# Kernel optimization log

Hardware: AMD Instinct MI355X
Metric: run time of the kernel (lower is better)

## Reference

```python
import jax, jax.numpy as jnp
import numpy as np

OBS, ACT, H, B = 128, 32, 64, 32768
TMAX = 8  # max variable-length GRU steps: (15-1)//2+1 == 15//2+1 == 8
CENTER = 7


def gru_last(x_seq, valid, Wih, Whh, bih, bhh):
    """torch nn.GRU cell, masked scan; returns final hidden at each true length.
    x_seq: (B, TMAX, D), valid: (B, TMAX) bool. Gate order r, z, n."""
    Bn = x_seq.shape[0]
    h0 = jnp.zeros((Bn, Whh.shape[1]), x_seq.dtype)

    def step(h, inp):
        xt, vt = inp  # (B, D), (B,)
        gi = xt @ Wih.T + bih
        gh = h @ Whh.T + bhh
        ir, iz, inn = jnp.split(gi, 3, axis=-1)
        hr, hz, hn = jnp.split(gh, 3, axis=-1)
        r = jax.nn.sigmoid(ir + hr)
        zg = jax.nn.sigmoid(iz + hz)
        n = jnp.tanh(inn + r * hn)
        hnew = (1.0 - zg) * n + zg * h
        h = jnp.where(vt[:, None], hnew, h)
        return h, None

    h, _ = jax.lax.scan(step, h0, (jnp.swapaxes(x_seq, 0, 1), valid.T))
    return h


def setup_inputs() -> dict:
    key = jax.random.key(0)
    ks = jax.random.split(key, 20)
    def p(k, shape, s=0.05):
        return jax.random.normal(k, shape, jnp.float32) * s
    D = OBS + ACT
    return dict(
        obs_chunk=jax.random.normal(ks[0], (B, 15, OBS), jnp.float32),
        act_chunk=jax.random.normal(ks[1], (B, 15, ACT), jnp.float32),
        ln_g=jnp.ones((3,), jnp.float32), ln_b=jnp.zeros((3,), jnp.float32),
        dw1=p(ks[2], (16, 3)), db1=jnp.zeros((16,), jnp.float32),
        dw2=p(ks[3], (8, 16)), db2=jnp.zeros((8,), jnp.float32),
        dw3=p(ks[4], (14, 8)), db3=jnp.zeros((14,), jnp.float32),
        Wih_f=p(ks[5], (3 * H, D)), Whh_f=p(ks[6], (3 * H, H)),
        bih_f=jnp.zeros((3 * H,), jnp.float32), bhh_f=jnp.zeros((3 * H,), jnp.float32),
        Wih_b=p(ks[7], (3 * H, D)), Whh_b=p(ks[8], (3 * H, H)),
        bih_b=jnp.zeros((3 * H,), jnp.float32), bhh_b=jnp.zeros((3 * H,), jnp.float32),
        mw1=p(ks[9], (H, 2 * H)), mb1=jnp.zeros((H,), jnp.float32),
        mw2=p(ks[10], (H, H)), mb2=jnp.zeros((H,), jnp.float32),
        mu_w=p(ks[11], (H, H)), mu_b=jnp.zeros((H,), jnp.float32),
        lv_w=p(ks[12], (H, H)), lv_b=jnp.zeros((H,), jnp.float32),
    )


def reference(obs_chunk, act_chunk, ln_g, ln_b, dw1, db1, dw2, db2, dw3, db3,
              Wih_f, Whh_f, bih_f, bhh_f, Wih_b, Whh_b, bih_b, bhh_b,
              mw1, mb1, mw2, mb2, mu_w, mu_b, lv_w, lv_b):
    C = CENTER
    # --- DynamicTimeWindow features ---
    obs_t = obs_chunk[:, C]  # (B, OBS)
    pr = jax.nn.softmax(obs_t, axis=-1)
    entropy = -jnp.sum(pr * jnp.log(pr + 1e-8), axis=-1, keepdims=True)
    diffs = jnp.stack([jnp.linalg.norm(obs_chunk[:, C - k] - obs_chunk[:, C - k - 1], axis=-1)
                       for k in range(3)], axis=1)
    roc = diffs.mean(axis=1, keepdims=True)
    act_prev = act_chunk[:, C - 1]
    md = max(obs_t.shape[-1], act_prev.shape[-1])
    op = jnp.pad(obs_t, ((0, 0), (0, md - obs_t.shape[-1])))
    ap = jnp.pad(act_prev, ((0, 0), (0, md - act_prev.shape[-1])))
    oc = op - op.mean(axis=1, keepdims=True)
    ac = ap - ap.mean(axis=1, keepdims=True)
    denom = (jnp.linalg.norm(oc, axis=1, keepdims=True)
             * jnp.linalg.norm(ac, axis=1, keepdims=True) + 1e-8)
    corr = jnp.sum(oc * ac, axis=1, keepdims=True) / denom
    f = jnp.concatenate([entropy, roc, corr], axis=1)  # (B, 3)
    mean = f.mean(axis=-1, keepdims=True)
    var = f.var(axis=-1, keepdims=True)  # biased, matches torch LayerNorm
    fn = (f - mean) / jnp.sqrt(var + 1e-5) * ln_g + ln_b
    h1 = jax.nn.relu(fn @ dw1.T + db1)
    h2 = jax.nn.relu(h1 @ dw2.T + db2)
    logits = h2 @ dw3.T + db3  # (B, 14)
    widx = jnp.argmax(logits, axis=1)  # test_mode: argmax of softmax == argmax of logits
    wl = widx + 2  # window_len in [2, 15]
    idxs = jnp.arange(15)[None, :]
    start = (C - (wl - 1) // 2)[:, None]
    end = (C + wl // 2 + 1)[:, None]
    mask = ((idxs >= start) & (idxs < end)).astype(obs_chunk.dtype)  # (B, 15)
    x = jnp.concatenate([obs_chunk, act_chunk], axis=-1) * mask[..., None]  # (B, 15, D)
    # --- BiGRU over variable-length windows ---
    len_f = (wl - 1) // 2 + 1  # (B,)
    len_b = wl // 2 + 1
    t = jnp.arange(TMAX)
    idx_f = C - len_f[:, None] + 1 + t[None, :]  # left-aligned forward window
    idx_b = C + len_b[:, None] - 1 - t[None, :]  # reversed backward window
    seq_f = jnp.take_along_axis(x, idx_f[..., None], axis=1)  # (B, 8, D)
    seq_b = jnp.take_along_axis(x, idx_b[..., None], axis=1)
    vf = t[None, :] < len_f[:, None]
    vb = t[None, :] < len_b[:, None]
    h_f = gru_last(seq_f, vf, Wih_f, Whh_f, bih_f, bhh_f)  # (B, H)
    h_b = gru_last(seq_b, vb, Wih_b, Whh_b, bih_b, bhh_b)
    comb = jnp.concatenate([h_f, h_b], axis=1)  # (B, 2H)
    zenc = jax.nn.relu(comb @ mw1.T + mb1) @ mw2.T + mb2
    mu = zenc @ mu_w.T + mu_b
    sigma = jnp.exp(0.5 * (zenc @ lv_w.T + lv_b))
    z = mu  # test_mode=True
    return (z, mu, sigma)
```

## Files before the change

kernel.cpp:

```cpp
#include <hip/hip_runtime.h>

#define OBS 128
#define ACTD 32
#define DIMX 160
#define HID 64
#define NBATCH 32768
#define TMAXX 8
#define CTR 7
#define NPOS 15

typedef short bf16x8 __attribute__((ext_vector_type(8)));
typedef float f32x4 __attribute__((ext_vector_type(4)));

#define MFMA(a,b,c) __builtin_amdgcn_mfma_f32_16x16x32_bf16((a),(b),(c),0,0,0)

#define CTRL_BYTE 262144
#define SIDX_BYTE 278528
#define SIDX_CAP  66048
#define WB_BYTE   542720
#define COMB_BYTE 755712
#define NCB 64
#define EPB 512
#define BH_OFF (40 + 1024)
#define HEAD_W_OFF 10752
#define TOTAL_SLOTS 13312

__device__ __forceinline__ unsigned short f2bf(float f) {
  unsigned u = __float_as_uint(f);
  return (unsigned short)((u + 0x7FFFu + ((u >> 16) & 1u)) >> 16);
}
__device__ __forceinline__ unsigned cvtpk(float a, float b) {
  unsigned r;
  asm("v_cvt_pk_bf16_f32 %0, %1, %2" : "=v"(r) : "v"(a), "v"(b));
  return r;
}

__device__ __forceinline__ float wsum(float v) {
#pragma unroll
  for (int s = 1; s < 64; s <<= 1) v += __shfl_xor(v, s);
  return v;
}
__device__ __forceinline__ float wmax(float v) {
#pragma unroll
  for (int s = 1; s < 64; s <<= 1) v = fmaxf(v, __shfl_xor(v, s));
  return v;
}

__global__ __launch_bounds__(256) void k_decide(
    const float* __restrict__ obs, const float* __restrict__ act,
    const float* __restrict__ ln_g, const float* __restrict__ ln_b,
    const float* __restrict__ dw1, const float* __restrict__ db1,
    const float* __restrict__ dw2, const float* __restrict__ db2,
    const float* __restrict__ dw3, const float* __restrict__ db3,
    int* __restrict__ lens) {
  int b = blockIdx.x * 4 + (threadIdx.x >> 6);
  int l = threadIdx.x & 63;
  const float* o7 = obs + ((size_t)b * NPOS + CTR) * OBS;
  const float* o6 = o7 - OBS;
  const float* o5 = o7 - 2 * OBS;
  const float* o4 = o7 - 3 * OBS;
  float x0 = o7[l], x1 = o7[l + 64];
  float y60 = o6[l], y61 = o6[l + 64];
  float y50 = o5[l], y51 = o5[l + 64];
  float y40 = o4[l], y41 = o4[l + 64];
  float ap = (l < 32) ? act[((size_t)b * NPOS + 6) * ACTD + l] : 0.0f;

  float m = wmax(fmaxf(x0, x1));
  float e0 = __expf(x0 - m), e1 = __expf(x1 - m);
  float s = wsum(e0 + e1);
  float dot = wsum(e0 * (x0 - m) + e1 * (x1 - m));
  float ent = __logf(s) - dot / s;

  float d0 = wsum((x0 - y60) * (x0 - y60) + (x1 - y61) * (x1 - y61));
  float d1 = wsum((y60 - y50) * (y60 - y50) + (y61 - y51) * (y61 - y51));
  float d2 = wsum((y50 - y40) * (y50 - y40) + (y51 - y41) * (y51 - y41));
  float roc = (sqrtf(d0) + sqrtf(d1) + sqrtf(d2)) / 3.0f;

  float sop = wsum(x0 + x1);
  float sop2 = wsum(x0 * x0 + x1 * x1);
  float sap = wsum(ap);
  float sap2 = wsum(ap * ap);
  float dotoa = wsum(ap * x0);
  float mo = sop / 128.0f, ma = sap / 128.0f;
  float num = dotoa - 128.0f * mo * ma;
  float oc2 = fmaxf(sop2 - 128.0f * mo * mo, 0.0f);
  float ac2 = fmaxf(sap2 - 128.0f * ma * ma, 0.0f);
  float corr = num / (sqrtf(oc2) * sqrtf(ac2) + 1e-8f);

  float f0 = ent, f1 = roc, f2 = corr;
  float mean = (f0 + f1 + f2) / 3.0f;
  float v0 = f0 - mean, v1 = f1 - mean, v2 = f2 - mean;
  float var = (v0 * v0 + v1 * v1 + v2 * v2) / 3.0f;
  float sd = sqrtf(var + 1e-5f);
  float fn0 = v0 / sd * ln_g[0] + ln_b[0];
  float fn1 = v1 / sd * ln_g[1] + ln_b[1];
  float fn2 = v2 / sd * ln_g[2] + ln_b[2];

  float h1[16];
#pragma unroll
  for (int i = 0; i < 16; i++) {
    float a = db1[i] + fn0 * dw1[i * 3] + fn1 * dw1[i * 3 + 1] + fn2 * dw1[i * 3 + 2];
    h1[i] = fmaxf(a, 0.0f);
  }
  float h2[8];
#pragma unroll
  for (int i = 0; i < 8; i++) {
    float a = db2[i];
#pragma unroll
    for (int j = 0; j < 16; j++) a += h1[j] * dw2[i * 16 + j];
    h2[i] = fmaxf(a, 0.0f);
  }
  float best = -3.0e38f;
  int bi = 0;
#pragma unroll
  for (int i = 0; i < 14; i++) {
    float a = db3[i];
#pragma unroll
    for (int j = 0; j < 8; j++) a += h2[j] * dw3[i * 8 + j];
    if (a > best) { best = a; bi = i; }
  }
  int wl = bi + 2;
  if (l == 0) {
    lens[b] = (wl - 1) / 2 + 1;
    lens[NBATCH + b] = wl / 2 + 1;
  }
}

__global__ __launch_bounds__(256) void k_cp(
    const int* __restrict__ lens, int* __restrict__ ctrl,
    const float* __restrict__ Wih_f, const float* __restrict__ Whh_f,
    const float* __restrict__ Wih_b, const float* __restrict__ Whh_b,
    const float* __restrict__ mw1, const float* __restrict__ mw2,
    const float* __restrict__ mu_w, const float* __restrict__ lv_w,
    unsigned short* __restrict__ dst) {
  __shared__ int hist[16];
  const int tid = threadIdx.x, blk = blockIdx.x;
  if (tid < 16) hist[tid] = 0;
  __syncthreads();
#pragma unroll
  for (int j = 0; j < 2; j++) {
    int e = blk * EPB + j * 256 + tid;
    atomicAdd(&hist[lens[e] - 1], 1);
    atomicAdd(&hist[8 + lens[NBATCH + e] - 1], 1);
  }
  {
    int slot = blk * 208 + (tid % 208) + (tid / 208) * 13312;
    if (tid < 208) {
      const float* src;
      if (slot < HEAD_W_OFF) {
        int d = slot / 5376, r = slot % 5376;
        int f = r >> 8, rw = r & 255;
        int w = rw >> 6, lane = rw & 63;
        int col = lane & 15, kgrp = lane >> 4;
        int row = 16 * w + col;
        if (f < 15) {
          int g = f / 5, kf = f % 5;
          const float* W = d ? Wih_b : Wih_f;
          src = W + (size_t)(g * 64 + row) * 160 + kf * 32 + kgrp * 8;
        } else {
          int f2 = f - 15, g = f2 >> 1, kh = f2 & 1;
          const float* W = d ? Whh_b : Whh_f;
          src = W + (size_t)(g * 64 + row) * 64 + kh * 32 + kgrp * 8;
        }
      } else {
        int s2 = slot - HEAD_W_OFF;
        int f = s2 >> 8, rw = s2 & 255;
        int w = rw >> 6, lane = rw & 63;
        int col = lane & 15, kgrp = lane >> 4;
        int gr = 16 * w + col;
        if (f < 4)      src = mw1 + (size_t)gr * 128 + f * 32 + kgrp * 8;
        else if (f < 6) src = mw2 + (size_t)gr * 64 + (f - 4) * 32 + kgrp * 8;
        else if (f < 8) src = mu_w + (size_t)gr * 64 + (f - 6) * 32 + kgrp * 8;
        else            src = lv_w + (size_t)gr * 64 + (f - 8) * 32 + kgrp * 8;
      }
      unsigned short* o = dst + (size_t)slot * 8;
#pragma unroll
      for (int i = 0; i < 8; i++) o[i] = f2bf(src[i]);
    }
  }
  __syncthreads();
  if (tid < 16) ctrl[BH_OFF + blk * 16 + tid] = hist[tid];
}

__global__ __launch_bounds__(256) void k_scanplace(
    const int* __restrict__ lens, int* __restrict__ ctrl,
    int* __restrict__ sidx) {
  __shared__ int hist[16];
  __shared__ int base[16];
  __shared__ int tot[16];
  __shared__ int pre[16];
  __shared__ int pss[17];
  __shared__ int border[16];
  __shared__ int bstart[16];
  const int tid = threadIdx.x, blk = blockIdx.x;
  const int* bh = ctrl + BH_OFF;
  if (tid < 16) {
    int t = 0, pr = 0;
    for (int b2 = 0; b2 < NCB; b2++) {
      int h = bh[b2 * 16 + tid];
      if (b2 < blk) pr += h;
      t += h;
    }
    tot[tid] = t;
    pre[tid] = pr;
    hist[tid] = 0;
  }
  __syncthreads();
  if (tid == 0) {
    int acc = 0;
    for (int r = 0; r < 16; r++) {
      int bin = (r & 1) * 8 + 7 - (r >> 1);
      border[r] = bin;
      pss[r] = acc;
      bstart[bin] = acc;
      acc += (tot[bin] + 31) & ~31;
    }
    pss[16] = acc;
    if (blk == 0) {
      for (int r = 0; r < 17; r++) ctrl[r] = pss[r];
      for (int r = 0; r < 16; r++) ctrl[17 + r] = border[r];
    }
  }
  __syncthreads();
  if (tid < 16) base[tid] = bstart[tid] + pre[tid];
  __syncthreads();
  if (blk == 0) {
    for (int r = 0; r < 16; r++) {
      int bin = border[r];
      int s = pss[r] + tot[bin], e2 = pss[r + 1];
      for (int i = s + tid; i < e2; i += 256) sidx[i] = -1;
    }
  }
#pragma unroll
  for (int j = 0; j < 2; j++) {
    int e = blk * EPB + j * 256 + tid;
    int binf = lens[e] - 1;
    sidx[base[binf] + atomicAdd(&hist[binf], 1)] = e;
    int binb = 8 + lens[NBATCH + e] - 1;
    sidx[base[binb] + atomicAdd(&hist[binb], 1)] = e;
  }
}

__global__ __launch_bounds__(256, 2) void k_gru(
    const float* __restrict__ obs, const float* __restrict__ act,
    const int* __restrict__ ctrl, const int* __restrict__ sidx,
    const unsigned short* __restrict__ wbf,
    const float* __restrict__ bih_f, const float* __restrict__ bhh_f,
    const float* __restrict__ bih_b, const float* __restrict__ bhh_b,
    unsigned short* __restrict__ comb) {
  __shared__ unsigned short Xl[2][32 * 168];
  __shared__ unsigned short Hl[2][32 * 72];
  __shared__ int ei[32];

  const int tid = threadIdx.x;
  const int p = blockIdx.x * 32;
  if (p >= ctrl[16]) return;
  int r = 0;
#pragma unroll
  for (int k = 1; k < 16; k++) r += (p >= ctrl[k]) ? 1 : 0;
  const int bin = ctrl[17 + r];
  const int d = bin >> 3;
  const int len = (bin & 7) + 1;

  if (tid < 32) ei[tid] = sidx[p + tid];
  __syncthreads();

  const int w = tid >> 6, l = tid & 63;
  const int col = l & 15, kgrp = l >> 4;
  const int gr = 16 * w + col;

  const float* bih = d ? bih_b : bih_f;
  const float* bhh = d ? bhh_b : bhh_f;
  const float bias_r = bih[gr] + bhh[gr];
  const float bias_z = bih[64 + gr] + bhh[64 + gr];
  const float bias_in = bih[128 + gr];
  const float bias_hn = bhh[128 + gr];

  const unsigned short* fb = wbf + ((size_t)d * 5376 + tid) * 8;
  bf16x8 wr[5], wz[5], wn[5];
#pragma unroll
  for (int kf = 0; kf < 5; kf++) {
    wr[kf] = *(const bf16x8*)(fb + (size_t)kf * 2048);
    wz[kf] = *(const bf16x8*)(fb + (size_t)(5 + kf) * 2048);
    wn[kf] = *(const bf16x8*)(fb + (size_t)(10 + kf) * 2048);
  }
  bf16x8 vr[2], vz[2], vn[2];
#pragma unroll
  for (int kh = 0; kh < 2; kh++) {
    vr[kh] = *(const bf16x8*)(fb + (size_t)(15 + kh) * 2048);
    vz[kh] = *(const bf16x8*)(fb + (size_t)(17 + kh) * 2048);
    vn[kh] = *(const bf16x8*)(fb + (size_t)(19 + kh) * 2048);
  }

  const int p0 = d ? (CTR + len - 1) : (CTR - len + 1);
  const float* pst[5];
  int sstr[5], sdo[5];
#pragma unroll
  for (int it = 0; it < 5; it++) {
    int i = tid + it * 256;
    int eloc = i / 40;
    int q = i - eloc * 40;
    int eg = ei[eloc];
    if (eg < 0) eg = ei[0];
    if (q < 32) {
      pst[it] = obs + ((size_t)eg * NPOS + p0) * OBS + q * 4;
      sstr[it] = d ? -OBS : OBS;
    } else {
      pst[it] = act + ((size_t)eg * NPOS + p0) * ACTD + (q - 32) * 4;
      sstr[it] = d ? -ACTD : ACTD;
    }
    sdo[it] = eloc * 168 + ((q < 32) ? q * 4 : 128 + (q - 32) * 4);
  }
  float4 sv[5];

  auto stage_issue = [&](int t1) {
#pragma unroll
    for (int it = 0; it < 5; it++)
      sv[it] = *(const float4*)(pst[it] + (ptrdiff_t)t1 * sstr[it]);
  };
  auto stage_commit = [&](int buf) {
#pragma unroll
    for (int it = 0; it < 5; it++) {
      uint2 pk;
      pk.x = cvtpk(sv[it].x, sv[it].y);
      pk.y = cvtpk(sv[it].z, sv[it].w);
      *(uint2*)(&Xl[buf][sdo[it]]) = pk;
    }
  };

  stage_issue(0);
  stage_commit(0);
  __syncthreads();

  f32x4 hreg[2];
#pragma unroll
  for (int m = 0; m < 2; m++) hreg[m] = (f32x4){0.f, 0.f, 0.f, 0.f};

  for (int t = 0; t < len; t++) {
    const int cur = t & 1, nxt = cur ^ 1;
    const bool more = (t + 1 < len);
    if (more) stage_issue(t + 1);

    f32x4 ar[2], az[2], ain[2], ahn[2];
#pragma unroll
    for (int m = 0; m < 2; m++) {
      ar[m] = (f32x4){bias_r, bias_r, bias_r, bias_r};
      az[m] = (f32x4){bias_z, bias_z, bias_z, bias_z};
      ain[m] = (f32x4){bias_in, bias_in, bias_in, bias_in};
      ahn[m] = (f32x4){bias_hn, bias_hn, bias_hn, bias_hn};
    }
#pragma unroll
    for (int kf = 0; kf < 5; kf++) {
#pragma unroll
      for (int m = 0; m < 2; m++) {
        bf16x8 xa = *(const bf16x8*)(&Xl[cur][(col + 16 * m) * 168 + kf * 32 + kgrp * 8]);
        ar[m] = MFMA(xa, wr[kf], ar[m]);
        az[m] = MFMA(xa, wz[kf], az[m]);
        ain[m] = MFMA(xa, wn[kf], ain[m]);
      }
    }
    if (t > 0) {
#pragma unroll
      for (int kh = 0; kh < 2; kh++) {
#pragma unroll
        for (int m = 0; m < 2; m++) {
          bf16x8 ha = *(const bf16x8*)(&Hl[cur][(col + 16 * m) * 72 + kh * 32 + kgrp * 8]);
          ar[m] = MFMA(ha, vr[kh], ar[m]);
          az[m] = MFMA(ha, vz[kh], az[m]);
          ahn[m] = MFMA(ha, vn[kh], ahn[m]);
        }
      }
    }

#pragma unroll
    for (int m = 0; m < 2; m++) {
      float hvv[4];
#pragma unroll
      for (int r2 = 0; r2 < 4; r2++) {
        float rg = __builtin_amdgcn_rcpf(1.0f + __expf(-ar[m][r2]));
        float zg = __builtin_amdgcn_rcpf(1.0f + __expf(-az[m][r2]));
        float nn = fmaf(rg, ahn[m][r2], ain[m][r2]);
        float th = fmaf(-2.0f, __builtin_amdgcn_rcpf(__expf(2.0f * nn) + 1.0f), 1.0f);
        float hp = hreg[m][r2];
        float hv = fmaf(zg, hp - th, th);
        hreg[m][r2] = hv;
        hvv[r2] = hv;
      }
      if (more) {
        unsigned ua = cvtpk(hvv[0], hvv[1]);
        unsigned ub = cvtpk(hvv[2], hvv[3]);
        int row0 = (16 * m + kgrp * 4) * 72 + gr;
        Hl[nxt][row0] = (unsigned short)ua;
        Hl[nxt][row0 + 72] = (unsigned short)(ua >> 16);
        Hl[nxt][row0 + 144] = (unsigned short)ub;
        Hl[nxt][row0 + 216] = (unsigned short)(ub >> 16);
      }
    }

    if (more) {
      stage_commit(nxt);
      __syncthreads();
    }
  }

#pragma unroll
  for (int m = 0; m < 2; m++) {
#pragma unroll
    for (int r2 = 0; r2 < 4; r2++) {
      int eg = ei[16 * m + kgrp * 4 + r2];
      if (eg >= 0)
        comb[(size_t)eg * 128 + 64 * d + gr] = f2bf(hreg[m][r2]);
    }
  }
}

__global__ __launch_bounds__(256) void k_head(
    const unsigned short* __restrict__ comb, const unsigned short* __restrict__ wbf,
    const float* __restrict__ mb1, const float* __restrict__ mb2,
    const float* __restrict__ mu_b, const float* __restrict__ lv_b,
    float* __restrict__ out) {
  __shared__ unsigned short Cl[64 * 136];
  __shared__ unsigned short Hl[64 * 72];
  __shared__ unsigned short Zl[64 * 72];

  const int tid = threadIdx.x;
  const int w = tid >> 6, l = tid & 63;
  const int col = l & 15, kgrp = l >> 4;
  const int gr = 16 * w + col;
  const int base = blockIdx.x * 64;

  {
    int row = tid >> 2, sq = tid & 3;
    const uint4* src = (const uint4*)(comb + (size_t)(base + row) * 128 + sq * 32);
    uint4* dst = (uint4*)(&Cl[row * 136 + sq * 32]);
#pragma unroll
    for (int j = 0; j < 4; j++) dst[j] = src[j];
  }
  __syncthreads();

  const unsigned short* hfb = wbf + ((size_t)HEAD_W_OFF + tid) * 8;
  const float b1 = mb1[gr], b2v = mb2[gr], bmu = mu_b[gr], blv = lv_b[gr];

  f32x4 t1[4];
#pragma unroll
  for (int m = 0; m < 4; m++) t1[m] = (f32x4){0.f, 0.f, 0.f, 0.f};
#pragma unroll
  for (int kf = 0; kf < 4; kf++) {
    bf16x8 bw = *(const bf16x8*)(hfb + (size_t)kf * 2048);
#pragma unroll
    for (int m = 0; m < 4; m++) {
      bf16x8 ca = *(const bf16x8*)(&Cl[(col + 16 * m) * 136 + kf * 32 + kgrp * 8]);
      t1[m] = MFMA(ca, bw, t1[m]);
    }
  }
#pragma unroll
  for (int m = 0; m < 4; m++) {
#pragma unroll
    for (int r = 0; r < 4; r++) {
      float v = fmaxf(t1[m][r] + b1, 0.0f);
      Hl[(16 * m + kgrp * 4 + r) * 72 + gr] = f2bf(v);
    }
  }
  __syncthreads();

  f32x4 ze[4];
#pragma unroll
  for (int m = 0; m < 4; m++) ze[m] = (f32x4){0.f, 0.f, 0.f, 0.f};
#pragma unroll
  for (int kh = 0; kh < 2; kh++) {
    bf16x8 bw = *(const bf16x8*)(hfb + (size_t)(4 + kh) * 2048);
#pragma unroll
    for (int m = 0; m < 4; m++) {
      bf16x8 ha = *(const bf16x8*)(&Hl[(col + 16 * m) * 72 + kh * 32 + kgrp * 8]);
      ze[m] = MFMA(ha, bw, ze[m]);
    }
  }
#pragma unroll
  for (int m = 0; m < 4; m++) {
#pragma unroll
    for (int r = 0; r < 4; r++) {
      Zl[(16 * m + kgrp * 4 + r) * 72 + gr] = f2bf(ze[m][r] + b2v);
    }
  }
  __syncthreads();

  f32x4 amu[4], alv[4];
#pragma unroll
  for (int m = 0; m < 4; m++) {
    amu[m] = (f32x4){0.f, 0.f, 0.f, 0.f};
    alv[m] = (f32x4){0.f, 0.f, 0.f, 0.f};
  }
#pragma unroll
  for (int kh = 0; kh < 2; kh++) {
    bf16x8 bwm = *(const bf16x8*)(hfb + (size_t)(6 + kh) * 2048);
    bf16x8 bwl = *(const bf16x8*)(hfb + (size_t)(8 + kh) * 2048);
#pragma unroll
    for (int m = 0; m < 4; m++) {
      bf16x8 za = *(const bf16x8*)(&Zl[(col + 16 * m) * 72 + kh * 32 + kgrp * 8]);
      amu[m] = MFMA(za, bwm, amu[m]);
      alv[m] = MFMA(za, bwl, alv[m]);
    }
  }
#pragma unroll
  for (int m = 0; m < 4; m++) {
#pragma unroll
    for (int r = 0; r < 4; r++) {
      int e = 16 * m + kgrp * 4 + r;
      float mu = amu[m][r] + bmu;
      float sg = expf(0.5f * (alv[m][r] + blv));
      size_t o = (size_t)(base + e) * HID + gr;
      out[o] = mu;
      out[(size_t)NBATCH * HID + o] = mu;
      out[2 * (size_t)NBATCH * HID + o] = sg;
    }
  }
}

extern "C" void kernel_launch(void* const* d_in, const int* in_sizes, int n_in,
                              void* d_out, int out_size, void* d_ws, size_t ws_size,
                              hipStream_t stream) {
  const float* obs = (const float*)d_in[0];
  const float* act = (const float*)d_in[1];
  const float* ln_g = (const float*)d_in[2];
  const float* ln_b = (const float*)d_in[3];
  const float* dw1 = (const float*)d_in[4];
  const float* db1 = (const float*)d_in[5];
  const float* dw2 = (const float*)d_in[6];
  const float* db2 = (const float*)d_in[7];
  const float* dw3 = (const float*)d_in[8];
  const float* db3 = (const float*)d_in[9];
  const float* Wih_f = (const float*)d_in[10];
  const float* Whh_f = (const float*)d_in[11];
  const float* bih_f = (const float*)d_in[12];
  const float* bhh_f = (const float*)d_in[13];
  const float* Wih_b = (const float*)d_in[14];
  const float* Whh_b = (const float*)d_in[15];
  const float* bih_b = (const float*)d_in[16];
  const float* bhh_b = (const float*)d_in[17];
  const float* mw1 = (const float*)d_in[18];
  const float* mb1 = (const float*)d_in[19];
  const float* mw2 = (const float*)d_in[20];
  const float* mb2 = (const float*)d_in[21];
  const float* mu_w = (const float*)d_in[22];
  const float* mu_b = (const float*)d_in[23];
  const float* lv_w = (const float*)d_in[24];
  const float* lv_b = (const float*)d_in[25];

  int* lens = (int*)d_ws;
  int* ctrl = (int*)((char*)d_ws + CTRL_BYTE);
  int* sidx = (int*)((char*)d_ws + SIDX_BYTE);
  unsigned short* wbf = (unsigned short*)((char*)d_ws + WB_BYTE);
  unsigned short* comb = (unsigned short*)((char*)d_ws + COMB_BYTE);

  k_decide<<<NBATCH / 4, 256, 0, stream>>>(obs, act, ln_g, ln_b, dw1, db1, dw2,
                                           db2, dw3, db3, lens);
  k_cp<<<NCB, 256, 0, stream>>>(lens, ctrl, Wih_f, Whh_f, Wih_b, Whh_b, mw1,
                                mw2, mu_w, lv_w, wbf);
  k_scanplace<<<NCB, 256, 0, stream>>>(lens, ctrl, sidx);
  k_gru<<<SIDX_CAP / 32, 256, 0, stream>>>(obs, act, ctrl, sidx, wbf, bih_f,
                                           bhh_f, bih_b, bhh_b, comb);
  k_head<<<NBATCH / 64, 256, 0, stream>>>(comb, wbf, mb1, mb2, mu_b, lv_b,
                                          (float*)d_out);
}
```

Before: 112.9 us.

## Stage GRU inputs with direct global-to-LDS loads and convert to bf16 at use

Replaces the register-staged global loads plus bf16 convert-and-store into LDS with asynchronous global_load_lds 16-byte transfers that place raw fp32 obs/act rows straight into padded LDS buffers. Conversion to bf16 now happens when MFMA operands are read from LDS. Gate accumulators are restructured per m-tile to cut live registers, and launch bounds are raised to 3 blocks per SM. The aim is to drop staging VGPRs and convert instructions from the prefetch path and raise occupancy. In exchange LDS traffic and footprint roughly double, and the convert work repeats on every read.

```diff
diff --git a/kernel.cpp b/kernel.cpp
--- a/kernel.cpp
+++ b/kernel.cpp
@@ -33,6 +33,11 @@
   unsigned r;
   asm("v_cvt_pk_bf16_f32 %0, %1, %2" : "=v"(r) : "v"(a), "v"(b));
   return r;
+}
+__device__ __forceinline__ void gload_lds16(const void* g, void* l) {
+  __builtin_amdgcn_global_load_lds(
+      (const __attribute__((address_space(1))) unsigned*)g,
+      (__attribute__((address_space(3))) unsigned*)l, 16, 0, 0);
 }
 
 __device__ __forceinline__ float wsum(float v) {
@@ -241,14 +246,15 @@
   }
 }
 
-__global__ __launch_bounds__(256, 2) void k_gru(
+__global__ __launch_bounds__(256, 3) void k_gru(
     const float* __restrict__ obs, const float* __restrict__ act,
     const int* __restrict__ ctrl, const int* __restrict__ sidx,
     const unsigned short* __restrict__ wbf,
     const float* __restrict__ bih_f, const float* __restrict__ bhh_f,
     const float* __restrict__ bih_b, const float* __restrict__ bhh_b,
     unsigned short* __restrict__ comb) {
-  __shared__ unsigned short Xl[2][32 * 168];
+  __shared__ float Xo[2][32 * 132 + 128];
+  __shared__ float Xa[2][32 * 36 + 128];
   __shared__ unsigned short Hl[2][32 * 72];
   __shared__ int ei[32];
 
@@ -265,9 +271,9 @@
   if (tid < 32) ei[tid] = sidx[p + tid];
   __syncthreads();
 
-  const int w = tid >> 6, l = tid & 63;
+  const int wv = tid >> 6, l = tid & 63;
   const int col = l & 15, kgrp = l >> 4;
-  const int gr = 16 * w + col;
+  const int gr = 16 * wv + col;
 
   const float* bih = d ? bih_b : bih_f;
   const float* bhh = d ? bhh_b : bhh_f;
@@ -293,43 +299,43 @@
   }
 
   const int p0 = d ? (CTR + len - 1) : (CTR - len + 1);
-  const float* pst[5];
-  int sstr[5], sdo[5];
-#pragma unroll
-  for (int it = 0; it < 5; it++) {
-    int i = tid + it * 256;
-    int eloc = i / 40;
-    int q = i - eloc * 40;
-    int eg = ei[eloc];
-    if (eg < 0) eg = ei[0];
-    if (q < 32) {
-      pst[it] = obs + ((size_t)eg * NPOS + p0) * OBS + q * 4;
-      sstr[it] = d ? -OBS : OBS;
-    } else {
-      pst[it] = act + ((size_t)eg * NPOS + p0) * ACTD + (q - 32) * 4;
-      sstr[it] = d ? -ACTD : ACTD;
-    }
-    sdo[it] = eloc * 168 + ((q < 32) ? q * 4 : 128 + (q - 32) * 4);
-  }
-  float4 sv[5];
-
-  auto stage_issue = [&](int t1) {
-#pragma unroll
-    for (int it = 0; it < 5; it++)
-      sv[it] = *(const float4*)(pst[it] + (ptrdiff_t)t1 * sstr[it]);
+  const int sOb = d ? -512 : 512;
+  const int sAb = d ? -128 : 128;
+  int offs[6];
+#pragma unroll
+  for (int j = 0; j < 6; j++) {
+    int c = wv + 4 * j;
+    offs[j] = 0;
+    if (c < 22) {
+      bool isO = c < 17;
+      int s16 = isO ? (c * 64 + l) : ((c - 17) * 64 + l);
+      int row, c16;
+      if (isO) { row = s16 / 33; c16 = (s16 % 33) & 31; }
+      else     { row = s16 / 9;  c16 = (s16 % 9) & 7; }
+      if (row > 31) row = 31;
+      int eg = ei[row];
+      if (eg < 0) eg = ei[0];
+      offs[j] = isO ? ((eg * 15 + p0) * 512 + c16 * 16)
+                    : ((eg * 15 + p0) * 128 + c16 * 16);
+    }
+  }
+
+  auto stage = [&](int buf, int t1) {
+#pragma unroll
+    for (int j = 0; j < 6; j++) {
+      int c = wv + 4 * j;
+      if (c < 22) {
+        bool isO = c < 17;
+        const char* src = (isO ? (const char*)obs : (const char*)act) +
+                          (ptrdiff_t)offs[j] + (ptrdiff_t)t1 * (isO ? sOb : sAb);
+        void* ldst = isO ? (void*)((char*)&Xo[buf][0] + c * 1024)
+                         : (void*)((char*)&Xa[buf][0] + (c - 17) * 1024);
+        gload_lds16(src, ldst);
+      }
+    }
   };
-  auto stage_commit = [&](int buf) {
-#pragma unroll
-    for (int it = 0; it < 5; it++) {
-      uint2 pk;
-      pk.x = cvtpk(sv[it].x, sv[it].y);
-      pk.y = cvtpk(sv[it].z, sv[it].w);
-      *(uint2*)(&Xl[buf][sdo[it]]) = pk;
-    }
-  };
-
-  stage_issue(0);
-  stage_commit(0);
+
+  stage(0, 0);
   __syncthreads();
 
   f32x4 hreg[2];
@@ -339,47 +345,46 @@
   for (int t = 0; t < len; t++) {
     const int cur = t & 1, nxt = cur ^ 1;
     const bool more = (t + 1 < len);
-    if (more) stage_issue(t + 1);
-
-    f32x4 ar[2], az[2], ain[2], ahn[2];
+    if (more) stage(nxt, t + 1);
+
 #pragma unroll
     for (int m = 0; m < 2; m++) {
-      ar[m] = (f32x4){bias_r, bias_r, bias_r, bias_r};
-      az[m] = (f32x4){bias_z, bias_z, bias_z, bias_z};
-      ain[m] = (f32x4){bias_in, bias_in, bias_in, bias_in};
-      ahn[m] = (f32x4){bias_hn, bias_hn, bias_hn, bias_hn};
-    }
-#pragma unroll
-    for (int kf = 0; kf < 5; kf++) {
-#pragma unroll
-      for (int m = 0; m < 2; m++) {
-        bf16x8 xa = *(const bf16x8*)(&Xl[cur][(col + 16 * m) * 168 + kf * 32 + kgrp * 8]);
-        ar[m] = MFMA(xa, wr[kf], ar[m]);
-        az[m] = MFMA(xa, wz[kf], az[m]);
-        ain[m] = MFMA(xa, wn[kf], ain[m]);
+      const int rr = col + 16 * m;
+      f32x4 ar = (f32x4){bias_r, bias_r, bias_r, bias_r};
+      f32x4 az = (f32x4){bias_z, bias_z, bias_z, bias_z};
+      f32x4 ain = (f32x4){bias_in, bias_in, bias_in, bias_in};
+      f32x4 ahn = (f32x4){bias_hn, bias_hn, bias_hn, bias_hn};
+#pragma unroll
+      for (int kf = 0; kf < 5; kf++) {
+        const float* xp = (kf < 4) ? &Xo[cur][rr * 132 + kf * 32 + kgrp * 8]
+                                   : &Xa[cur][rr * 36 + kgrp * 8];
+        float4 a0 = *(const float4*)xp;
+        float4 a1 = *(const float4*)(xp + 4);
+        bf16x8 xa;
+        unsigned* xu = (unsigned*)&xa;
+        xu[0] = cvtpk(a0.x, a0.y);
+        xu[1] = cvtpk(a0.z, a0.w);
+        xu[2] = cvtpk(a1.x, a1.y);
+        xu[3] = cvtpk(a1.z, a1.w);
+        ar = MFMA(xa, wr[kf], ar);
+        az = MFMA(xa, wz[kf], az);
+        ain = MFMA(xa, wn[kf], ain);
       }
-    }
-    if (t > 0) {
-#pragma unroll
-      for (int kh = 0; kh < 2; kh++) {
-#pragma unroll
-        for (int m = 0; m < 2; m++) {
-          bf16x8 ha = *(const bf16x8*)(&Hl[cur][(col + 16 * m) * 72 + kh * 32 + kgrp * 8]);
-          ar[m] = MFMA(ha, vr[kh], ar[m]);
-          az[m] = MFMA(ha, vz[kh], az[m]);
-          ahn[m] = MFMA(ha, vn[kh], ahn[m]);
+      if (t > 0) {
+#pragma unroll
+        for (int kh = 0; kh < 2; kh++) {
+          bf16x8 ha = *(const bf16x8*)(&Hl[cur][rr * 72 + kh * 32 + kgrp * 8]);
+          ar = MFMA(ha, vr[kh], ar);
+          az = MFMA(ha, vz[kh], az);
+          ahn = MFMA(ha, vn[kh], ahn);
         }
       }
-    }
-
-#pragma unroll
-    for (int m = 0; m < 2; m++) {
       float hvv[4];
 #pragma unroll
       for (int r2 = 0; r2 < 4; r2++) {
-        float rg = __builtin_amdgcn_rcpf(1.0f + __expf(-ar[m][r2]));
-        float zg = __builtin_amdgcn_rcpf(1.0f + __expf(-az[m][r2]));
-        float nn = fmaf(rg, ahn[m][r2], ain[m][r2]);
+        float rg = __builtin_amdgcn_rcpf(1.0f + __expf(-ar[r2]));
+        float zg = __builtin_amdgcn_rcpf(1.0f + __expf(-az[r2]));
+        float nn = fmaf(rg, ahn[r2], ain[r2]);
         float th = fmaf(-2.0f, __builtin_amdgcn_rcpf(__expf(2.0f * nn) + 1.0f), 1.0f);
         float hp = hreg[m][r2];
         float hv = fmaf(zg, hp - th, th);
@@ -397,10 +402,7 @@
       }
     }
 
-    if (more) {
-      stage_commit(nxt);
-      __syncthreads();
-    }
+    if (more) __syncthreads();
   }
 
 #pragma unroll
```

Measured after the change: 133.9 us. 1.19x slower.
